# Kernel optimization log

Hardware: AMD Instinct MI355X
Metric: run time of the kernel (lower is better)

## Reference

```python
import jax, jax.numpy as jnp
import numpy as np

B, S, NB = 8, 512, 23
INIT, E, R, T = 512, 256, 3, 2
NEG = -9e8

def _gru(x, h, wih, whh, bih, bhh):
    gi = x @ wih.T + bih
    gh = h @ whh.T + bhh
    ir, iz, inn = jnp.split(gi, 3, axis=-1)
    hr, hz, hn = jnp.split(gh, 3, axis=-1)
    r = jax.nn.sigmoid(ir + hr)
    z = jax.nn.sigmoid(iz + hz)
    n = jnp.tanh(inn + r * hn)
    return (1.0 - z) * n + z * h

def setup_inputs():
    key = jax.random.key(0)
    ks = jax.random.split(key, 30)
    def lin(k, o, i):
        return jax.random.normal(k, (o, i), jnp.float32) * 0.02
    def vec(k, n):
        return jax.random.normal(k, (n,), jnp.float32) * 0.02
    inp = {}
    inp["amino_list"] = jax.random.normal(ks[0], (B, S, INIT), jnp.float32)
    inp["amino_mask"] = (jax.random.uniform(ks[1], (B, S)) < 0.9).astype(jnp.float32)
    inp["emb_W"] = lin(ks[2], E, INIT); inp["emb_b"] = vec(ks[3], E)
    inp["nb_W"] = lin(ks[4], E, INIT); inp["nb_b"] = vec(ks[5], E)
    inp["align_W"] = jax.random.normal(ks[6], (R, 1, 2 * E), jnp.float32) * 0.02
    inp["align_b"] = jax.random.normal(ks[7], (R, 1), jnp.float32) * 0.02
    inp["attend_W"] = jax.random.normal(ks[8], (R, E, E), jnp.float32) * 0.02
    inp["attend_b"] = jax.random.normal(ks[9], (R, E), jnp.float32) * 0.02
    inp["gru_wih"] = jax.random.normal(ks[10], (R, 3 * E, E), jnp.float32) * 0.02
    inp["gru_whh"] = jax.random.normal(ks[11], (R, 3 * E, E), jnp.float32) * 0.02
    inp["gru_bih"] = jax.random.normal(ks[12], (R, 3 * E), jnp.float32) * 0.02
    inp["gru_bhh"] = jax.random.normal(ks[13], (R, 3 * E), jnp.float32) * 0.02
    inp["seq_align_W"] = lin(ks[14], 1, 2 * E); inp["seq_align_b"] = vec(ks[15], 1)
    inp["seq_attend_W"] = lin(ks[16], E, E); inp["seq_attend_b"] = vec(ks[17], E)
    inp["seq_gru_wih"] = lin(ks[18], 3 * E, E); inp["seq_gru_bih"] = vec(ks[19], 3 * E)
    inp["seq_gru_whh"] = lin(ks[20], 3 * E, E); inp["seq_gru_bhh"] = vec(ks[21], 3 * E)
    inp["amino_degree_list"] = jax.random.randint(ks[22], (B, S, NB), -1, S)
    return inp

def reference(amino_list, amino_mask, emb_W, emb_b, nb_W, nb_b, align_W, align_b,
              attend_W, attend_b, gru_wih, gru_whh, gru_bih, gru_bhh,
              seq_align_W, seq_align_b, seq_attend_W, seq_attend_b,
              seq_gru_wih, seq_gru_whh, seq_gru_bih, seq_gru_bhh, amino_degree_list):
    idx = amino_degree_list
    lrelu = jax.nn.leaky_relu
    # per-batch neighbor gather: (S,D),(S,NB) -> (S,NB,D); index -1 wraps (masked out below)
    gather = jax.vmap(lambda f, i: f[i])
    feat = lrelu(amino_list @ emb_W.T + emb_b)               # (B,S,E)
    nfeat = lrelu(gather(amino_list, idx) @ nb_W.T + nb_b)   # (B,S,NB,E)
    attend_mask = (idx != -1).astype(feat.dtype)             # (B,S,NB)
    smask = jnp.where(idx == -1, NEG, 0.0).astype(feat.dtype)

    def attn(d, center, nbr):
        # align Linear on concat([center, nbr]) split into two matvecs (same math, no concat)
        aW = align_W[d, 0]
        score = lrelu(jnp.einsum('bse,e->bs', center, aW[:E])[:, :, None]
                      + jnp.einsum('bsne,e->bsn', nbr, aW[E:]) + align_b[d, 0])
        w = jax.nn.softmax(score + smask, axis=-1) * attend_mask   # softmax over neighbor axis
        nt = nbr @ attend_W[d].T + attend_b[d]
        return jax.nn.elu(jnp.einsum('bsn,bsne->bse', w, nt))

    h = _gru(attn(0, feat, nfeat).reshape(-1, E), feat.reshape(-1, E),
             gru_wih[0], gru_whh[0], gru_bih[0], gru_bhh[0])
    act = jax.nn.relu(h.reshape(B, S, E))
    for d in range(1, R):
        ctx = attn(d, act, gather(act, idx))
        h = _gru(ctx.reshape(-1, E), h, gru_wih[d], gru_whh[d], gru_bih[d], gru_bhh[d])
        act = jax.nn.relu(h.reshape(B, S, E))

    seq_feature = jnp.sum(act * amino_mask[:, :, None], axis=1)  # (B,E)
    act_mol = jax.nn.relu(seq_feature)                           # fixed across T (as in torch)
    seq_smask = jnp.where(amino_mask == 0, NEG, 0.0)
    saW = seq_align_W[0]
    act_seq = act_mol
    for _ in range(T):
        score = lrelu((act_mol @ saW[:E])[:, None]
                      + jnp.einsum('bse,e->bs', act, saW[E:]) + seq_align_b[0])
        w = jax.nn.softmax(score + seq_smask, axis=-1) * amino_mask  # softmax over seq axis
        tf = act @ seq_attend_W.T + seq_attend_b
        seq_ctx = jax.nn.elu(jnp.einsum('bs,bse->be', w, tf))
        seq_feature = _gru(seq_ctx, seq_feature, seq_gru_wih, seq_gru_whh, seq_gru_bih, seq_gru_bhh)
        act_seq = jax.nn.relu(seq_feature)
    return (act_seq, act)
```

## Files before the change

kernel.cpp:

```cpp
#include <hip/hip_runtime.h>
#include <math.h>


#define BSZ   8
#define SEQ   512
#define NBR   23
#define EMB   256
#define INITD 512
#define BS    (BSZ*SEQ)
#define G3    (3*EMB)
#define NEGV  -9e8f

typedef __attribute__((ext_vector_type(8))) short short8;
typedef __attribute__((ext_vector_type(4))) float f32x4;

__device__ __forceinline__ float lrelu(float x){ return x > 0.f ? x : 0.01f*x; }
__device__ __forceinline__ float elu1 (float x){ return x > 0.f ? x : (expf(x)-1.f); }
__device__ __forceinline__ float sigm (float x){ return 1.f/(1.f+expf(-x)); }
__device__ __forceinline__ float bf2f(ushort u){
    union { unsigned int i; float f; } v; v.i = ((unsigned int)u) << 16; return v.f;
}
__device__ __forceinline__ ushort f2bf(float f){
    union { float f; unsigned int i; } v; v.f = f;
    unsigned int u = v.i;
    return (ushort)((u + 0x7FFFu + ((u >> 16) & 1u)) >> 16);
}

struct GemmLds { ushort A[2][64][64]; ushort W[2][64][64]; };

__global__ __launch_bounds__(256) void convert9_kernel(
    const float* s0, ushort* d0, int n0,
    const float* s1, ushort* d1, int n1,
    const float* s2, ushort* d2, int n2,
    const float* s3, ushort* d3, int n3,
    const float* s4, ushort* d4, int n4,
    const float* s5, ushort* d5, int n5,
    const float* s6, ushort* d6, int n6,
    const float* s7, ushort* d7, int n7,
    const float* s8, ushort* d8, int n8)
{
    const float* srcs[9] = {s0,s1,s2,s3,s4,s5,s6,s7,s8};
    ushort* dsts[9] = {d0,d1,d2,d3,d4,d5,d6,d7,d8};
    int ns[9] = {n0,n1,n2,n3,n4,n5,n6,n7,n8};
    int seg = blockIdx.y;
    const float* s = srcs[seg]; ushort* d = dsts[seg]; int n = ns[seg];
    size_t i = ((size_t)blockIdx.x * 256 + threadIdx.x) * 8;
    size_t stride = (size_t)gridDim.x * 256 * 8;
    for (; i < (size_t)n; i += stride) {
        float4 a = *reinterpret_cast<const float4*>(s + i);
        float4 b = *reinterpret_cast<const float4*>(s + i + 4);
        uint4 o;
        o.x = (unsigned)f2bf(a.x) | ((unsigned)f2bf(a.y) << 16);
        o.y = (unsigned)f2bf(a.z) | ((unsigned)f2bf(a.w) << 16);
        o.z = (unsigned)f2bf(b.x) | ((unsigned)f2bf(b.y) << 16);
        o.w = (unsigned)f2bf(b.z) | ((unsigned)f2bf(b.w) << 16);
        *reinterpret_cast<uint4*>(d + i) = o;
    }
}

template<int ACT, bool WF32, bool WBF>
__device__ __forceinline__ void gemm_dev(
    const ushort* __restrict__ A, const ushort* __restrict__ W,
    const float* __restrict__ bias,
    float* __restrict__ C, ushort* __restrict__ Cbf,
    int N, int K, int bx, int by, GemmLds& L)
{
    const int tid = threadIdx.x;
    const int m0 = bx * 64, n0 = by * 64;
    const int wv = tid >> 6, lane = tid & 63;
    const int fr = lane & 15, grp = lane >> 4;
    const int lrow = tid >> 3, lc8 = tid & 7;
    const int kc = K >> 3;
    const int sw = lc8 ^ (lrow & 7);

    f32x4 acc[4];
    #pragma unroll
    for (int c = 0; c < 4; ++c) acc[c] = (f32x4){0.f, 0.f, 0.f, 0.f};

    const float4* A4 = reinterpret_cast<const float4*>(A);
    const float4* W4 = reinterpret_cast<const float4*>(W);

    float4 a0 = A4[(size_t)(m0 + lrow)      * kc + lc8];
    float4 a1 = A4[(size_t)(m0 + lrow + 32) * kc + lc8];
    float4 w0 = W4[(size_t)(n0 + lrow)      * kc + lc8];
    float4 w1 = W4[(size_t)(n0 + lrow + 32) * kc + lc8];
    *reinterpret_cast<float4*>(&L.A[0][lrow     ][sw << 3]) = a0;
    *reinterpret_cast<float4*>(&L.A[0][lrow + 32][sw << 3]) = a1;
    *reinterpret_cast<float4*>(&L.W[0][lrow     ][sw << 3]) = w0;
    *reinterpret_cast<float4*>(&L.W[0][lrow + 32][sw << 3]) = w1;
    __syncthreads();

    const int ar = (wv << 4) + fr;
    int cur = 0;
    for (int k0 = 64; k0 < K; k0 += 64) {
        a0 = A4[(size_t)(m0 + lrow)      * kc + (k0 >> 3) + lc8];
        a1 = A4[(size_t)(m0 + lrow + 32) * kc + (k0 >> 3) + lc8];
        w0 = W4[(size_t)(n0 + lrow)      * kc + (k0 >> 3) + lc8];
        w1 = W4[(size_t)(n0 + lrow + 32) * kc + (k0 >> 3) + lc8];
        #pragma unroll
        for (int ks = 0; ks < 2; ++ks) {
            short8 af = *reinterpret_cast<const short8*>(
                &L.A[cur][ar][((((ks << 2) + grp) ^ (ar & 7)) << 3)]);
            #pragma unroll
            for (int c = 0; c < 4; ++c) {
                const int br = (c << 4) + fr;
                short8 bv = *reinterpret_cast<const short8*>(
                    &L.W[cur][br][((((ks << 2) + grp) ^ (br & 7)) << 3)]);
                acc[c] = __builtin_amdgcn_mfma_f32_16x16x32_bf16(af, bv, acc[c], 0, 0, 0);
            }
        }
        *reinterpret_cast<float4*>(&L.A[cur^1][lrow     ][sw << 3]) = a0;
        *reinterpret_cast<float4*>(&L.A[cur^1][lrow + 32][sw << 3]) = a1;
        *reinterpret_cast<float4*>(&L.W[cur^1][lrow     ][sw << 3]) = w0;
        *reinterpret_cast<float4*>(&L.W[cur^1][lrow + 32][sw << 3]) = w1;
        __syncthreads();
        cur ^= 1;
    }
    #pragma unroll
    for (int ks = 0; ks < 2; ++ks) {
        short8 af = *reinterpret_cast<const short8*>(
            &L.A[cur][ar][((((ks << 2) + grp) ^ (ar & 7)) << 3)]);
        #pragma unroll
        for (int c = 0; c < 4; ++c) {
            const int br = (c << 4) + fr;
            short8 bv = *reinterpret_cast<const short8*>(
                &L.W[cur][br][((((ks << 2) + grp) ^ (br & 7)) << 3)]);
            acc[c] = __builtin_amdgcn_mfma_f32_16x16x32_bf16(af, bv, acc[c], 0, 0, 0);
        }
    }

    const int mrow = m0 + (wv << 4) + (grp << 2);
    #pragma unroll
    for (int c = 0; c < 4; ++c) {
        const int n = n0 + (c << 4) + fr;
        const float bv = bias[n];
        #pragma unroll
        for (int j = 0; j < 4; ++j) {
            float t = acc[c][j] + bv;
            if (ACT == 1) t = lrelu(t);
            size_t off = (size_t)(mrow + j) * N + n;
            if (WF32) C[off] = t;
            if (WBF)  Cbf[off] = f2bf(t);
        }
    }
}

template<int ACT, bool WF32, bool WBF>
__global__ __launch_bounds__(256) void gemm_mfma(
    const ushort* __restrict__ A, const ushort* __restrict__ W,
    const float* __restrict__ bias,
    float* __restrict__ C, ushort* __restrict__ Cbf, int N, int K)
{
    __shared__ GemmLds L;
    gemm_dev<ACT,WF32,WBF>(A, W, bias, C, Cbf, N, K, blockIdx.x, blockIdx.y, L);
}

__global__ __launch_bounds__(256) void featnbase_kernel(
    const ushort* __restrict__ aminobf,
    const ushort* __restrict__ embWbf, const float* __restrict__ embB,
    float* __restrict__ feat, ushort* __restrict__ featbf,
    const ushort* __restrict__ nbWbf, const float* __restrict__ nbB,
    float* __restrict__ nbase, ushort* __restrict__ nbasebf)
{
    __shared__ GemmLds L;
    int blk = blockIdx.x;
    if (blk < 256)
        gemm_dev<1,true,true>(aminobf, embWbf, embB, feat, featbf, EMB, INITD, blk & 63, blk >> 6, L);
    else {
        blk -= 256;
        gemm_dev<1,true,true>(aminobf, nbWbf, nbB, nbase, nbasebf, EMB, INITD, blk & 63, blk >> 6, L);
    }
}

__global__ __launch_bounds__(256) void round_pre_kernel(
    const ushort* __restrict__ nbrbf, const ushort* __restrict__ attWd,
    const float* __restrict__ attBd, ushort* __restrict__ ntb,
    const ushort* __restrict__ hprevbf, const ushort* __restrict__ gwhhd,
    const float* __restrict__ gbhhd, ushort* __restrict__ ghbf,
    const float* __restrict__ center, const float* __restrict__ nbrbase,
    const float* __restrict__ alignWd,
    float* __restrict__ cdot, float* __restrict__ ndot)
{
    __shared__ GemmLds L;
    int blk = blockIdx.x;
    if (blk < 256) {
        gemm_dev<0,false,true>(nbrbf, attWd, attBd, nullptr, ntb, EMB, EMB, blk & 63, blk >> 6, L);
    } else if (blk < 1024) {
        int b = blk - 256;
        gemm_dev<0,false,true>(hprevbf, gwhhd, gbhhd, nullptr, ghbf, G3, EMB, b & 63, b >> 6, L);
    } else {
        const int b    = blk - 1024;
        const int lane = threadIdx.x & 63;
        const int wv   = threadIdx.x >> 6;
        const int e    = lane << 2;
        const int rb   = b * 16 + wv * 4;
        float4 w0 = *reinterpret_cast<const float4*>(&alignWd[e]);
        float4 w1 = *reinterpret_cast<const float4*>(&alignWd[EMB + e]);
        #pragma unroll
        for (int i = 0; i < 4; ++i) {
            const int r = rb + i;
            float4 xc = *reinterpret_cast<const float4*>(&center[(size_t)r*EMB + e]);
            float4 xn = *reinterpret_cast<const float4*>(&nbrbase[(size_t)r*EMB + e]);
            float ac = xc.x*w0.x + xc.y*w0.y + xc.z*w0.z + xc.w*w0.w;
            float an = xn.x*w1.x + xn.y*w1.y + xn.z*w1.z + xn.w*w1.w;
            #pragma unroll
            for (int off = 32; off; off >>= 1) {
                ac += __shfl_xor(ac, off, 64);
                an += __shfl_xor(an, off, 64);
            }
            if (lane == 0) { cdot[r] = ac; ndot[r] = an; }
        }
    }
}

__global__ __launch_bounds__(256) void attn_kernel(
    const float* __restrict__ cdot, const float* __restrict__ ndot,
    const int* __restrict__ idx, const ushort* __restrict__ nt,
    const float* __restrict__ alignB, ushort* __restrict__ ctxbf)
{
    const int lane = threadIdx.x & 63;
    const int r = blockIdx.x * 4 + (threadIdx.x >> 6);
    const int b = r >> 9;
    float sc = -3e38f, vm = 0.f; int row = 0;
    if (lane < NBR) {
        int j = idx[(size_t)r*NBR + lane];
        int valid = (j >= 0);
        int jj = valid ? j : j + SEQ;
        row = b*SEQ + jj;
        vm = (float)valid;
        sc = lrelu(cdot[r] + ndot[row] + alignB[0]) + (valid ? 0.f : NEGV);
    }
    float m = sc;
    #pragma unroll
    for (int off = 32; off; off >>= 1) m = fmaxf(m, __shfl_xor(m, off, 64));
    float ev = (lane < NBR) ? expf(sc - m) : 0.f;
    float s = ev;
    #pragma unroll
    for (int off = 32; off; off >>= 1) s += __shfl_xor(s, off, 64);
    float wgt = ev * vm / s;
    float acc0 = 0.f, acc1 = 0.f, acc2 = 0.f, acc3 = 0.f;
    const int e = lane << 2;
    #pragma unroll 1
    for (int n = 0; n < NBR; ++n) {
        float wn = __shfl(wgt, n, 64);
        int   rn = __shfl(row, n, 64);
        ushort4 v = *reinterpret_cast<const ushort4*>(&nt[(size_t)rn*EMB + e]);
        acc0 += wn * bf2f(v.x); acc1 += wn * bf2f(v.y);
        acc2 += wn * bf2f(v.z); acc3 += wn * bf2f(v.w);
    }
    uint2 o;
    o.x = (unsigned)f2bf(elu1(acc0)) | ((unsigned)f2bf(elu1(acc1)) << 16);
    o.y = (unsigned)f2bf(elu1(acc2)) | ((unsigned)f2bf(elu1(acc3)) << 16);
    *reinterpret_cast<uint2*>(&ctxbf[(size_t)r*EMB + e]) = o;
}

__global__ __launch_bounds__(256) void gru_kernel(
    const ushort* __restrict__ gibf, const ushort* __restrict__ ghbf,
    const float* __restrict__ hprev,
    float* __restrict__ hout, ushort* __restrict__ hbf,
    float* __restrict__ actout, ushort* __restrict__ actbf)
{
    const size_t r = blockIdx.x * 4 + (threadIdx.x >> 6);
    const int    e = (threadIdx.x & 63) << 2;
    const size_t gb = r*G3 + e, hb = r*EMB + e;
    ushort4 ir4 = *reinterpret_cast<const ushort4*>(&gibf[gb]);
    ushort4 iz4 = *reinterpret_cast<const ushort4*>(&gibf[gb + EMB]);
    ushort4 in4 = *reinterpret_cast<const ushort4*>(&gibf[gb + 2*EMB]);
    ushort4 hr4 = *reinterpret_cast<const ushort4*>(&ghbf[gb]);
    ushort4 hz4 = *reinterpret_cast<const ushort4*>(&ghbf[gb + EMB]);
    ushort4 hn4 = *reinterpret_cast<const ushort4*>(&ghbf[gb + 2*EMB]);
    float4 hp4 = *reinterpret_cast<const float4*>(&hprev[hb]);
    const float ir_[4] = {bf2f(ir4.x),bf2f(ir4.y),bf2f(ir4.z),bf2f(ir4.w)};
    const float iz_[4] = {bf2f(iz4.x),bf2f(iz4.y),bf2f(iz4.z),bf2f(iz4.w)};
    const float in_[4] = {bf2f(in4.x),bf2f(in4.y),bf2f(in4.z),bf2f(in4.w)};
    const float hr_[4] = {bf2f(hr4.x),bf2f(hr4.y),bf2f(hr4.z),bf2f(hr4.w)};
    const float hz_[4] = {bf2f(hz4.x),bf2f(hz4.y),bf2f(hz4.z),bf2f(hz4.w)};
    const float hn_[4] = {bf2f(hn4.x),bf2f(hn4.y),bf2f(hn4.z),bf2f(hn4.w)};
    const float hp_[4] = {hp4.x,hp4.y,hp4.z,hp4.w};
    float hv[4], av[4];
    #pragma unroll
    for (int i = 0; i < 4; ++i) {
        float rg = sigm(ir_[i] + hr_[i]);
        float z  = sigm(iz_[i] + hz_[i]);
        float n  = tanhf(in_[i] + rg*hn_[i]);
        hv[i] = (1.f - z)*n + z*hp_[i];
        av[i] = fmaxf(hv[i], 0.f);
    }
    *reinterpret_cast<float4*>(&hout[hb])   = make_float4(hv[0],hv[1],hv[2],hv[3]);
    *reinterpret_cast<float4*>(&actout[hb]) = make_float4(av[0],av[1],av[2],av[3]);
    uint2 hp, ap;
    hp.x = (unsigned)f2bf(hv[0]) | ((unsigned)f2bf(hv[1]) << 16);
    hp.y = (unsigned)f2bf(hv[2]) | ((unsigned)f2bf(hv[3]) << 16);
    ap.x = (unsigned)f2bf(av[0]) | ((unsigned)f2bf(av[1]) << 16);
    ap.y = (unsigned)f2bf(av[2]) | ((unsigned)f2bf(av[3]) << 16);
    *reinterpret_cast<uint2*>(&hbf[hb])   = hp;
    *reinterpret_cast<uint2*>(&actbf[hb]) = ap;
}

__global__ __launch_bounds__(256) void seqpre_kernel(
    const ushort* __restrict__ actbf, const ushort* __restrict__ satWbf,
    const float* __restrict__ satB, float* __restrict__ tf,
    const float* __restrict__ act, const float* __restrict__ mask,
    const float* __restrict__ saW,
    float* __restrict__ seqfeat, float* __restrict__ cmol,
    float* __restrict__ ad)
{
    __shared__ GemmLds L;
    int blk = blockIdx.x;
    if (blk < 256) {
        gemm_dev<0,true,false>(actbf, satWbf, satB, tf, nullptr, EMB, EMB, blk & 63, blk >> 6, L);
    } else if (blk < 264) {
        const int b = blk - 256;
        const int e = threadIdx.x;
        float acc = 0.f;
        for (int s = 0; s < SEQ; ++s)
            acc += act[((size_t)b*SEQ + s)*EMB + e] * mask[b*SEQ + s];
        seqfeat[b*EMB + e] = acc;
        float* red = reinterpret_cast<float*>(&L);
        red[e] = fmaxf(acc, 0.f) * saW[e];
        __syncthreads();
        for (int off = 128; off; off >>= 1) {
            if (e < off) red[e] += red[e + off];
            __syncthreads();
        }
        if (e == 0) cmol[b] = red[0];
    } else {
        const int b2   = blk - 264;
        const int lane = threadIdx.x & 63;
        const int wv   = threadIdx.x >> 6;
        const int e    = lane << 2;
        const int rb   = b2 * 16 + wv * 4;
        float4 w1 = *reinterpret_cast<const float4*>(&saW[EMB + e]);
        #pragma unroll
        for (int i = 0; i < 4; ++i) {
            const int r = rb + i;
            float4 xa = *reinterpret_cast<const float4*>(&act[(size_t)r*EMB + e]);
            float an = xa.x*w1.x + xa.y*w1.y + xa.z*w1.z + xa.w*w1.w;
            #pragma unroll
            for (int off = 32; off; off >>= 1) an += __shfl_xor(an, off, 64);
            if (lane == 0) ad[r] = an;
        }
    }
}

__global__ __launch_bounds__(256) void seqpv2_kernel(
    const float* __restrict__ ad, const float* __restrict__ mask,
    const float* __restrict__ saB, const float* __restrict__ cmol,
    const float* __restrict__ tf, float* __restrict__ partial)
{
    const int st = blockIdx.x, b = blockIdx.y;
    const int tid = threadIdx.x;
    __shared__ float w_s[SEQ];
    __shared__ float red[256];
    float mk0 = mask[b*SEQ + tid], mk1 = mask[b*SEQ + 256 + tid];
    float cb = cmol[b], bb = saB[0];
    float s0 = lrelu(cb + ad[b*SEQ + tid] + bb)       + (mk0 == 0.f ? NEGV : 0.f);
    float s1 = lrelu(cb + ad[b*SEQ + 256 + tid] + bb) + (mk1 == 0.f ? NEGV : 0.f);
    red[tid] = fmaxf(s0, s1); __syncthreads();
    for (int off = 128; off; off >>= 1) {
        if (tid < off) red[tid] = fmaxf(red[tid], red[tid + off]);
        __syncthreads();
    }
    float m = red[0]; __syncthreads();
    float e0 = expf(s0 - m), e1 = expf(s1 - m);
    red[tid] = e0 + e1; __syncthreads();
    for (int off = 128; off; off >>= 1) {
        if (tid < off) red[tid] += red[tid + off];
        __syncthreads();
    }
    float inv = 1.f / red[0];
    w_s[tid]       = e0 * inv * mk0;
    w_s[tid + 256] = e1 * inv * mk1;
    __syncthreads();
    float acc = 0.f;
    const int s0i = st * 32;
    #pragma unroll 4
    for (int s = s0i; s < s0i + 32; ++s)
        acc += w_s[s] * tf[((size_t)b*SEQ + s)*EMB + tid];
    partial[((size_t)b*16 + st)*EMB + tid] = acc;
}

template<int T0>
__global__ __launch_bounds__(512) void seqstep_kernel(
    const float* __restrict__ partial, const float* __restrict__ sfin,
    const ushort* __restrict__ sgwihbf, const float* __restrict__ sgbih,
    const ushort* __restrict__ sgwhhbf, const float* __restrict__ sgbhh,
    float* __restrict__ sgi, float* __restrict__ sfout,
    float* __restrict__ actseq)
{
    const int b = blockIdx.x >> 2, q = blockIdx.x & 3;
    const int tid = threadIdx.x, lane = tid & 63, wv = tid >> 6;
    __shared__ float xs[EMB];
    __shared__ float hs[EMB];
    __shared__ float gis[192], ghs[192];
    if (tid < EMB) {
        hs[tid] = sfin[b*EMB + tid];
        if (T0) {
            float a = 0.f;
            #pragma unroll
            for (int st = 0; st < 16; ++st)
                a += partial[((size_t)b*16 + st)*EMB + tid];
            xs[tid] = elu1(a);
        }
    }
    if (!T0) {
        for (int l = tid; l < 192; l += 512) {
            int g = (l >> 6)*EMB + (q << 6) + (l & 63);
            gis[l] = sgi[b*G3 + g];
        }
    }
    __syncthreads();
    const int nrows = T0 ? 384 : 192;
    const int rpw = nrows >> 3;
    for (int i = 0; i < rpw; ++i) {
        const int l = wv * rpw + i;
        const int iswih = T0 && (l < 192);
        const int ll = (T0 && l >= 192) ? l - 192 : l;
        const int g = (ll >> 6)*EMB + (q << 6) + (ll & 63);
        const ushort* Wm = iswih ? sgwihbf : sgwhhbf;
        ushort4 w4 = *reinterpret_cast<const ushort4*>(&Wm[(size_t)g*EMB + (lane << 2)]);
        float4 x4 = *reinterpret_cast<const float4*>(iswih ? &xs[lane << 2] : &hs[lane << 2]);
        float d = bf2f(w4.x)*x4.x + bf2f(w4.y)*x4.y + bf2f(w4.z)*x4.z + bf2f(w4.w)*x4.w;
        #pragma unroll
        for (int off = 32; off; off >>= 1) d += __shfl_xor(d, off, 64);
        if (lane == 0) {
            if (iswih) {
                d += sgbih[g];
                gis[ll] = d;
                sgi[b*G3 + g] = d;
            } else {
                ghs[ll] = d + sgbhh[g];
            }
        }
    }
    __syncthreads();
    if (tid < 64) {
        const int e = (q << 6) + tid;
        float rg = sigm(gis[tid]       + ghs[tid]);
        float z  = sigm(gis[64 + tid]  + ghs[64 + tid]);
        float n  = tanhf(gis[128 + tid] + rg*ghs[128 + tid]);
        float hv = (1.f - z)*n + z*hs[e];
        sfout[b*EMB + e]  = hv;
        actseq[b*EMB + e] = fmaxf(hv, 0.f);
    }
}

extern "C" void kernel_launch(void* const* d_in, const int* in_sizes, int n_in,
                              void* d_out, int out_size, void* d_ws, size_t ws_size,
                              hipStream_t stream) {
    (void)in_sizes; (void)n_in; (void)out_size; (void)ws_size;
    const float* amino  = (const float*)d_in[0];
    const float* mask   = (const float*)d_in[1];
    const float* embW   = (const float*)d_in[2];
    const float* embB   = (const float*)d_in[3];
    const float* nbW    = (const float*)d_in[4];
    const float* nbB    = (const float*)d_in[5];
    const float* alignW = (const float*)d_in[6];
    const float* alignB = (const float*)d_in[7];
    const float* attW   = (const float*)d_in[8];
    const float* attB   = (const float*)d_in[9];
    const float* gwih   = (const float*)d_in[10];
    const float* gwhh   = (const float*)d_in[11];
    const float* gbih   = (const float*)d_in[12];
    const float* gbhh   = (const float*)d_in[13];
    const float* saW    = (const float*)d_in[14];
    const float* saB    = (const float*)d_in[15];
    const float* satW   = (const float*)d_in[16];
    const float* satB   = (const float*)d_in[17];
    const float* sgwih  = (const float*)d_in[18];
    const float* sgbih  = (const float*)d_in[19];
    const float* sgwhh  = (const float*)d_in[20];
    const float* sgbhh  = (const float*)d_in[21];
    const int*   idx    = (const int*)d_in[22];

    char* cur = (char*)d_ws;
    auto alloc = [&](size_t bytes) -> char* {
        char* p = cur; cur += (bytes + 255) & ~(size_t)255; return p;
    };
    float* feat    = (float*)alloc((size_t)BS*EMB*4);
    float* nbase   = (float*)alloc((size_t)BS*EMB*4);
    float* h       = (float*)alloc((size_t)BS*EMB*4);
    float* tf      = (float*)alloc((size_t)BS*EMB*4);
    float* cdot    = (float*)alloc(BS*4);
    float* ndot    = (float*)alloc(BS*4);
    float* ad      = (float*)alloc(BS*4);
    float* seqfeat = (float*)alloc(BSZ*EMB*4);
    float* sf2     = (float*)alloc(BSZ*EMB*4);
    float* cmol    = (float*)alloc(64*4);
    float* sgi     = (float*)alloc(BSZ*G3*4);
    float* partial = (float*)alloc((size_t)BSZ*16*EMB*4);
    ushort* aminobf = (ushort*)alloc((size_t)BS*INITD*2);
    ushort* featbf  = (ushort*)alloc((size_t)BS*EMB*2);
    ushort* nbasebf = (ushort*)alloc((size_t)BS*EMB*2);
    ushort* actbf   = (ushort*)alloc((size_t)BS*EMB*2);
    ushort* hbf     = (ushort*)alloc((size_t)BS*EMB*2);
    ushort* ctxbf   = (ushort*)alloc((size_t)BS*EMB*2);
    ushort* ntb     = (ushort*)alloc((size_t)BS*EMB*2);
    ushort* gibf    = (ushort*)alloc((size_t)BS*G3*2);
    ushort* ghbf    = (ushort*)alloc((size_t)BS*G3*2);
    ushort* embWbf  = (ushort*)alloc((size_t)EMB*INITD*2);
    ushort* nbWbf   = (ushort*)alloc((size_t)EMB*INITD*2);
    ushort* attWbf  = (ushort*)alloc((size_t)3*EMB*EMB*2);
    ushort* gwihbf  = (ushort*)alloc((size_t)3*G3*EMB*2);
    ushort* gwhhbf  = (ushort*)alloc((size_t)3*G3*EMB*2);
    ushort* satWbf  = (ushort*)alloc((size_t)EMB*EMB*2);
    ushort* sgwihbf = (ushort*)alloc((size_t)G3*EMB*2);
    ushort* sgwhhbf = (ushort*)alloc((size_t)G3*EMB*2);

    float* out    = (float*)d_out;
    float* actseq = out;
    float* act    = out + BSZ*EMB;

    convert9_kernel<<<dim3(1024, 9), 256, 0, stream>>>(
        amino, aminobf, BS*INITD,
        embW,  embWbf,  EMB*INITD,
        nbW,   nbWbf,   EMB*INITD,
        attW,  attWbf,  3*EMB*EMB,
        gwih,  gwihbf,  3*G3*EMB,
        gwhh,  gwhhbf,  3*G3*EMB,
        satW,  satWbf,  EMB*EMB,
        sgwih, sgwihbf, G3*EMB,
        sgwhh, sgwhhbf, G3*EMB);

    featnbase_kernel<<<512, 256, 0, stream>>>(
        aminobf, embWbf, embB, feat, featbf, nbWbf, nbB, nbase, nbasebf);

    for (int d = 0; d < 3; ++d) {
        const float*  center   = (d == 0) ? feat    : act;
        const float*  nbrbase  = (d == 0) ? nbase   : act;
        const ushort* nbrbf    = (d == 0) ? nbasebf : actbf;
        const float*  hprev    = (d == 0) ? feat    : h;
        const ushort* hprevbf  = (d == 0) ? featbf  : hbf;
        round_pre_kernel<<<1280, 256, 0, stream>>>(
            nbrbf, attWbf + (size_t)d*EMB*EMB, attB + d*EMB, ntb,
            hprevbf, gwhhbf + (size_t)d*G3*EMB, gbhh + d*G3, ghbf,
            center, nbrbase, alignW + d*2*EMB, cdot, ndot);
        attn_kernel<<<BS/4, 256, 0, stream>>>(cdot, ndot, idx, ntb, alignB + d, ctxbf);
        gemm_mfma<0,false,true><<<dim3(64, 12), 256, 0, stream>>>(
            ctxbf, gwihbf + (size_t)d*G3*EMB, gbih + d*G3, nullptr, gibf, G3, EMB);
        gru_kernel<<<BS/4, 256, 0, stream>>>(gibf, ghbf, hprev, h, hbf, act, actbf);
    }

    seqpre_kernel<<<520, 256, 0, stream>>>(
        actbf, satWbf, satB, tf, act, mask, saW, seqfeat, cmol, ad);
    seqpv2_kernel<<<dim3(16, BSZ), 256, 0, stream>>>(ad, mask, saB, cmol, tf, partial);
    seqstep_kernel<1><<<32, 512, 0, stream>>>(
        partial, seqfeat, sgwihbf, sgbih, sgwhhbf, sgbhh, sgi, sf2, actseq);
    seqstep_kernel<0><<<32, 512, 0, stream>>>(
        partial, sf2, sgwihbf, sgbih, sgwhhbf, sgbhh, sgi, seqfeat, actseq);
}
```

Before: 187.8 us.

## Use larger GEMM tiles with direct global-to-LDS loads

Reworks the shared GEMM device routine to use 128-row tiles (and 64- or 128-column tiles), with each wave computing a 4xFN block of MFMA outputs. Operand tiles are staged with global_load_lds instead of passing through registers. Grid sizes for every fused kernel shrink to match, and the auxiliary dot-product blocks now handle 32 rows each. The larger tiles give more reuse per LDS load but leave fewer blocks on a large GPU, so occupancy may drop and wave-level parallelism may be lower.

```diff
diff --git a/kernel.cpp b/kernel.cpp
--- a/kernel.cpp
+++ b/kernel.cpp
@@ -26,7 +26,17 @@
     return (ushort)((u + 0x7FFFu + ((u >> 16) & 1u)) >> 16);
 }
 
-struct GemmLds { ushort A[2][64][64]; ushort W[2][64][64]; };
+__device__ __forceinline__ void gload_lds16(const void* g, void* l) {
+    __builtin_amdgcn_global_load_lds(
+        (const __attribute__((address_space(1))) unsigned int*)g,
+        (__attribute__((address_space(3))) unsigned int*)l,
+        16, 0, 0);
+}
+
+template<int BN> struct GemmLdsT {
+    ushort A[2][128][64];
+    ushort B[2][BN][64];
+};
 
 __global__ __launch_bounds__(256) void convert9_kernel(
     const float* s0, ushort* d0, int n0,
@@ -58,101 +68,108 @@
     }
 }
 
-template<int ACT, bool WF32, bool WBF>
+template<int BN, int ACT, bool WF32, bool WBF>
 __device__ __forceinline__ void gemm_dev(
     const ushort* __restrict__ A, const ushort* __restrict__ W,
     const float* __restrict__ bias,
     float* __restrict__ C, ushort* __restrict__ Cbf,
-    int N, int K, int bx, int by, GemmLds& L)
-{
+    int N, int K, int bx, int by, GemmLdsT<BN>& L)
+{
+    constexpr int FN = BN / 32;
     const int tid = threadIdx.x;
-    const int m0 = bx * 64, n0 = by * 64;
+    const int m0 = bx * 128, n0 = by * BN;
     const int wv = tid >> 6, lane = tid & 63;
     const int fr = lane & 15, grp = lane >> 4;
-    const int lrow = tid >> 3, lc8 = tid & 7;
     const int kc = K >> 3;
-    const int sw = lc8 ^ (lrow & 7);
-
-    f32x4 acc[4];
+    const int mh = wv & 1, nh = wv >> 1;
+    const int lrow = lane >> 3;
+    const int csrc = (lane & 7) ^ lrow;
+
+    f32x4 acc[4][FN];
     #pragma unroll
-    for (int c = 0; c < 4; ++c) acc[c] = (f32x4){0.f, 0.f, 0.f, 0.f};
-
-    const float4* A4 = reinterpret_cast<const float4*>(A);
-    const float4* W4 = reinterpret_cast<const float4*>(W);
-
-    float4 a0 = A4[(size_t)(m0 + lrow)      * kc + lc8];
-    float4 a1 = A4[(size_t)(m0 + lrow + 32) * kc + lc8];
-    float4 w0 = W4[(size_t)(n0 + lrow)      * kc + lc8];
-    float4 w1 = W4[(size_t)(n0 + lrow + 32) * kc + lc8];
-    *reinterpret_cast<float4*>(&L.A[0][lrow     ][sw << 3]) = a0;
-    *reinterpret_cast<float4*>(&L.A[0][lrow + 32][sw << 3]) = a1;
-    *reinterpret_cast<float4*>(&L.W[0][lrow     ][sw << 3]) = w0;
-    *reinterpret_cast<float4*>(&L.W[0][lrow + 32][sw << 3]) = w1;
+    for (int i = 0; i < 4; ++i)
+        #pragma unroll
+        for (int n = 0; n < FN; ++n) acc[i][n] = (f32x4){0.f,0.f,0.f,0.f};
+
+    auto stage = [&](int c, int k0) {
+        const int kch = (k0 >> 3) + csrc;
+        #pragma unroll
+        for (int i = 0; i < 4; ++i) {
+            const int s = (wv << 2) + i;
+            const ushort* g = A + ((size_t)(m0 + (s << 3) + lrow) * kc + kch) * 8;
+            gload_lds16(g, &L.A[c][s << 3][0]);
+        }
+        #pragma unroll
+        for (int i = 0; i < FN; ++i) {
+            const int s = wv * FN + i;
+            const ushort* g = W + ((size_t)(n0 + (s << 3) + lrow) * kc + kch) * 8;
+            gload_lds16(g, &L.B[c][s << 3][0]);
+        }
+    };
+
+    auto compute = [&](int c) {
+        #pragma unroll
+        for (int ks = 0; ks < 2; ++ks) {
+            short8 af[4];
+            #pragma unroll
+            for (int i = 0; i < 4; ++i) {
+                const int ar = (mh << 6) + (i << 4) + fr;
+                af[i] = *reinterpret_cast<const short8*>(
+                    &L.A[c][ar][(((ks << 2) + grp) ^ (ar & 7)) << 3]);
+            }
+            #pragma unroll
+            for (int n = 0; n < FN; ++n) {
+                const int br = nh * (BN/2) + (n << 4) + fr;
+                short8 bv = *reinterpret_cast<const short8*>(
+                    &L.B[c][br][(((ks << 2) + grp) ^ (br & 7)) << 3]);
+                #pragma unroll
+                for (int i = 0; i < 4; ++i)
+                    acc[i][n] = __builtin_amdgcn_mfma_f32_16x16x32_bf16(
+                        af[i], bv, acc[i][n], 0, 0, 0);
+            }
+        }
+    };
+
+    const int KT = K >> 6;
+    stage(0, 0);
     __syncthreads();
-
-    const int ar = (wv << 4) + fr;
     int cur = 0;
-    for (int k0 = 64; k0 < K; k0 += 64) {
-        a0 = A4[(size_t)(m0 + lrow)      * kc + (k0 >> 3) + lc8];
-        a1 = A4[(size_t)(m0 + lrow + 32) * kc + (k0 >> 3) + lc8];
-        w0 = W4[(size_t)(n0 + lrow)      * kc + (k0 >> 3) + lc8];
-        w1 = W4[(size_t)(n0 + lrow + 32) * kc + (k0 >> 3) + lc8];
-        #pragma unroll
-        for (int ks = 0; ks < 2; ++ks) {
-            short8 af = *reinterpret_cast<const short8*>(
-                &L.A[cur][ar][((((ks << 2) + grp) ^ (ar & 7)) << 3)]);
-            #pragma unroll
-            for (int c = 0; c < 4; ++c) {
-                const int br = (c << 4) + fr;
-                short8 bv = *reinterpret_cast<const short8*>(
-                    &L.W[cur][br][((((ks << 2) + grp) ^ (br & 7)) << 3)]);
-                acc[c] = __builtin_amdgcn_mfma_f32_16x16x32_bf16(af, bv, acc[c], 0, 0, 0);
-            }
-        }
-        *reinterpret_cast<float4*>(&L.A[cur^1][lrow     ][sw << 3]) = a0;
-        *reinterpret_cast<float4*>(&L.A[cur^1][lrow + 32][sw << 3]) = a1;
-        *reinterpret_cast<float4*>(&L.W[cur^1][lrow     ][sw << 3]) = w0;
-        *reinterpret_cast<float4*>(&L.W[cur^1][lrow + 32][sw << 3]) = w1;
+    for (int kt = 1; kt < KT; ++kt) {
+        stage(cur ^ 1, kt << 6);
+        compute(cur);
         __syncthreads();
         cur ^= 1;
     }
+    compute(cur);
+
     #pragma unroll
-    for (int ks = 0; ks < 2; ++ks) {
-        short8 af = *reinterpret_cast<const short8*>(
-            &L.A[cur][ar][((((ks << 2) + grp) ^ (ar & 7)) << 3)]);
-        #pragma unroll
-        for (int c = 0; c < 4; ++c) {
-            const int br = (c << 4) + fr;
-            short8 bv = *reinterpret_cast<const short8*>(
-                &L.W[cur][br][((((ks << 2) + grp) ^ (br & 7)) << 3)]);
-            acc[c] = __builtin_amdgcn_mfma_f32_16x16x32_bf16(af, bv, acc[c], 0, 0, 0);
-        }
-    }
-
-    const int mrow = m0 + (wv << 4) + (grp << 2);
-    #pragma unroll
-    for (int c = 0; c < 4; ++c) {
-        const int n = n0 + (c << 4) + fr;
-        const float bv = bias[n];
-        #pragma unroll
-        for (int j = 0; j < 4; ++j) {
-            float t = acc[c][j] + bv;
-            if (ACT == 1) t = lrelu(t);
-            size_t off = (size_t)(mrow + j) * N + n;
-            if (WF32) C[off] = t;
-            if (WBF)  Cbf[off] = f2bf(t);
+    for (int i = 0; i < 4; ++i) {
+        const int mrow = m0 + (mh << 6) + (i << 4) + (grp << 2);
+        #pragma unroll
+        for (int n = 0; n < FN; ++n) {
+            const int col = n0 + nh * (BN/2) + (n << 4) + fr;
+            const float bv = bias[col];
+            #pragma unroll
+            for (int j = 0; j < 4; ++j) {
+                float t = acc[i][n][j] + bv;
+                if (ACT == 1) t = lrelu(t);
+                size_t off = (size_t)(mrow + j) * N + col;
+                if (WF32) C[off] = t;
+                if (WBF)  Cbf[off] = f2bf(t);
+            }
         }
     }
 }
 
 template<int ACT, bool WF32, bool WBF>
-__global__ __launch_bounds__(256) void gemm_mfma(
+__global__ __launch_bounds__(256) void gemm_mfma128(
     const ushort* __restrict__ A, const ushort* __restrict__ W,
     const float* __restrict__ bias,
     float* __restrict__ C, ushort* __restrict__ Cbf, int N, int K)
 {
-    __shared__ GemmLds L;
-    gemm_dev<ACT,WF32,WBF>(A, W, bias, C, Cbf, N, K, blockIdx.x, blockIdx.y, L);
+    __shared__ GemmLdsT<128> L;
+    gemm_dev<128,ACT,WF32,WBF>(A, W, bias, C, Cbf, N, K,
+                               blockIdx.x & 31, blockIdx.x >> 5, L);
 }
 
 __global__ __launch_bounds__(256) void featnbase_kernel(
@@ -162,13 +179,15 @@
     const ushort* __restrict__ nbWbf, const float* __restrict__ nbB,
     float* __restrict__ nbase, ushort* __restrict__ nbasebf)
 {
-    __shared__ GemmLds L;
+    __shared__ GemmLdsT<64> L;
     int blk = blockIdx.x;
-    if (blk < 256)
-        gemm_dev<1,true,true>(aminobf, embWbf, embB, feat, featbf, EMB, INITD, blk & 63, blk >> 6, L);
+    if (blk < 128)
+        gemm_dev<64,1,true,true>(aminobf, embWbf, embB, feat, featbf,
+                                 EMB, INITD, blk & 31, blk >> 5, L);
     else {
-        blk -= 256;
-        gemm_dev<1,true,true>(aminobf, nbWbf, nbB, nbase, nbasebf, EMB, INITD, blk & 63, blk >> 6, L);
+        blk -= 128;
+        gemm_dev<64,1,true,true>(aminobf, nbWbf, nbB, nbase, nbasebf,
+                                 EMB, INITD, blk & 31, blk >> 5, L);
     }
 }
 
@@ -181,23 +200,25 @@
     const float* __restrict__ alignWd,
     float* __restrict__ cdot, float* __restrict__ ndot)
 {
-    __shared__ GemmLds L;
+    __shared__ GemmLdsT<128> L;
     int blk = blockIdx.x;
-    if (blk < 256) {
-        gemm_dev<0,false,true>(nbrbf, attWd, attBd, nullptr, ntb, EMB, EMB, blk & 63, blk >> 6, L);
-    } else if (blk < 1024) {
-        int b = blk - 256;
-        gemm_dev<0,false,true>(hprevbf, gwhhd, gbhhd, nullptr, ghbf, G3, EMB, b & 63, b >> 6, L);
+    if (blk < 64) {
+        gemm_dev<128,0,false,true>(nbrbf, attWd, attBd, nullptr, ntb,
+                                   EMB, EMB, blk & 31, blk >> 5, L);
+    } else if (blk < 256) {
+        int b = blk - 64;
+        gemm_dev<128,0,false,true>(hprevbf, gwhhd, gbhhd, nullptr, ghbf,
+                                   G3, EMB, b & 31, b >> 5, L);
     } else {
-        const int b    = blk - 1024;
+        const int b    = blk - 256;
         const int lane = threadIdx.x & 63;
         const int wv   = threadIdx.x >> 6;
         const int e    = lane << 2;
-        const int rb   = b * 16 + wv * 4;
+        const int rb   = b * 32 + wv * 8;
         float4 w0 = *reinterpret_cast<const float4*>(&alignWd[e]);
         float4 w1 = *reinterpret_cast<const float4*>(&alignWd[EMB + e]);
         #pragma unroll
-        for (int i = 0; i < 4; ++i) {
+        for (int i = 0; i < 8; ++i) {
             const int r = rb + i;
             float4 xc = *reinterpret_cast<const float4*>(&center[(size_t)r*EMB + e]);
             float4 xn = *reinterpret_cast<const float4*>(&nbrbase[(size_t)r*EMB + e]);
@@ -305,12 +326,13 @@
     float* __restrict__ seqfeat, float* __restrict__ cmol,
     float* __restrict__ ad)
 {
-    __shared__ GemmLds L;
+    __shared__ GemmLdsT<64> L;
     int blk = blockIdx.x;
-    if (blk < 256) {
-        gemm_dev<0,true,false>(actbf, satWbf, satB, tf, nullptr, EMB, EMB, blk & 63, blk >> 6, L);
-    } else if (blk < 264) {
-        const int b = blk - 256;
+    if (blk < 128) {
+        gemm_dev<64,0,true,false>(actbf, satWbf, satB, tf, nullptr,
+                                  EMB, EMB, blk & 31, blk >> 5, L);
+    } else if (blk < 136) {
+        const int b = blk - 128;
         const int e = threadIdx.x;
         float acc = 0.f;
         for (int s = 0; s < SEQ; ++s)
@@ -325,14 +347,14 @@
         }
         if (e == 0) cmol[b] = red[0];
     } else {
-        const int b2   = blk - 264;
+        const int b2   = blk - 136;
         const int lane = threadIdx.x & 63;
         const int wv   = threadIdx.x >> 6;
         const int e    = lane << 2;
-        const int rb   = b2 * 16 + wv * 4;
+        const int rb   = b2 * 32 + wv * 8;
         float4 w1 = *reinterpret_cast<const float4*>(&saW[EMB + e]);
         #pragma unroll
-        for (int i = 0; i < 4; ++i) {
+        for (int i = 0; i < 8; ++i) {
             const int r = rb + i;
             float4 xa = *reinterpret_cast<const float4*>(&act[(size_t)r*EMB + e]);
             float an = xa.x*w1.x + xa.y*w1.y + xa.z*w1.z + xa.w*w1.w;
@@ -522,7 +544,7 @@
         sgwih, sgwihbf, G3*EMB,
         sgwhh, sgwhhbf, G3*EMB);
 
-    featnbase_kernel<<<512, 256, 0, stream>>>(
+    featnbase_kernel<<<256, 256, 0, stream>>>(
         aminobf, embWbf, embB, feat, featbf, nbWbf, nbB, nbase, nbasebf);
 
     for (int d = 0; d < 3; ++d) {
@@ -531,17 +553,17 @@
         const ushort* nbrbf    = (d == 0) ? nbasebf : actbf;
         const float*  hprev    = (d == 0) ? feat    : h;
         const ushort* hprevbf  = (d == 0) ? featbf  : hbf;
-        round_pre_kernel<<<1280, 256, 0, stream>>>(
+        round_pre_kernel<<<384, 256, 0, stream>>>(
             nbrbf, attWbf + (size_t)d*EMB*EMB, attB + d*EMB, ntb,
             hprevbf, gwhhbf + (size_t)d*G3*EMB, gbhh + d*G3, ghbf,
             center, nbrbase, alignW + d*2*EMB, cdot, ndot);
         attn_kernel<<<BS/4, 256, 0, stream>>>(cdot, ndot, idx, ntb, alignB + d, ctxbf);
-        gemm_mfma<0,false,true><<<dim3(64, 12), 256, 0, stream>>>(
+        gemm_mfma128<0,false,true><<<192, 256, 0, stream>>>(
             ctxbf, gwihbf + (size_t)d*G3*EMB, gbih + d*G3, nullptr, gibf, G3, EMB);
         gru_kernel<<<BS/4, 256, 0, stream>>>(gibf, ghbf, hprev, h, hbf, act, actbf);
     }
 
-    seqpre_kernel<<<520, 256, 0, stream>>>(
+    seqpre_kernel<<<264, 256, 0, stream>>>(
         actbf, satWbf, satB, tf, act, mask, saW, seqfeat, cmol, ad);
     seqpv2_kernel<<<dim3(16, BSZ), 256, 0, stream>>>(ad, mask, saB, cmol, tf, partial);
     seqstep_kernel<1><<<32, 512, 0, stream>>>(
```

Result: no change. 191.0 us (+1.7%).
